# Performance work log

Hardware: AMD Instinct MI355X
Metric: run time of the kernel (lower is better)

The kernel has to match this reference:

```python
import jax, jax.numpy as jnp
import numpy as np

BATCH = 2
SEQ = 2048
DIM = 2048
HEADS = 16
DIM_HEAD = 64
DIM_INNER = HEADS * DIM_HEAD  # 1024
SOFTCAP = 50.0
EPS = 1e-12


def setup_inputs() -> dict:
    key = jax.random.key(0)
    k1, k2, k3, k4 = jax.random.split(key, 4)
    x = jax.random.normal(k1, (BATCH, SEQ, DIM), dtype=jnp.float32)
    # RMSNorm gamma param (initialized near zero in the torch module)
    gamma = jax.random.normal(k2, (DIM,), dtype=jnp.float32) * 0.02
    # Linear weights stored already-transposed: x @ W
    w_qkv = jax.random.normal(k3, (DIM, 3 * DIM_INNER), dtype=jnp.float32) * (DIM ** -0.5)
    w_out = jax.random.normal(k4, (DIM_INNER, DIM), dtype=jnp.float32) * (DIM_INNER ** -0.5)
    # (type, offset, length) triples per batch; bidirectional attention inside each span
    modalities = jnp.array(
        [[[0, 256, 256], [0, 1024, 512]],
         [[0, 128, 256], [0, 1536, 384]]], dtype=jnp.int32)
    return dict(x=x, gamma=gamma, w_qkv=w_qkv, w_out=w_out, modalities=modalities)


def _transfusion_attn_mask(seq_len, modalities):
    # causal | (q in span AND kv in span)  -> Bool[b, i, j]
    seq = jnp.arange(seq_len)
    causal = seq[:, None] >= seq[None, :]                      # [i, j]
    offsets = modalities[..., 1]                                # [b, m]
    ends = offsets + modalities[..., 2]                         # [b, m]
    q_in = seq[None, None, :] >= offsets[..., None]             # [b, m, i]
    kv_in = seq[None, None, :] < ends[..., None]                # [b, m, j]
    is_modality = jnp.any(q_in[..., :, None] & kv_in[..., None, :], axis=1)  # [b, i, j]
    return causal[None] | is_modality


def _rmsnorm(x, gamma):
    n = jnp.sqrt(jnp.sum(x * x, axis=-1, keepdims=True))
    x = x / jnp.maximum(n, EPS)
    return x * (DIM ** 0.5) * (gamma + 1.0)


def reference(x, gamma, w_qkv, w_out, modalities):
    xn = _rmsnorm(x, gamma)
    qkv = xn @ w_qkv                                            # [b, n, 3*h*d]
    qkv = qkv.reshape(BATCH, SEQ, 3, HEADS, DIM_HEAD)
    qkv = jnp.transpose(qkv, (2, 0, 3, 1, 4))                   # [3, b, h, n, d]
    q, k, v = qkv[0], qkv[1], qkv[2]
    q = q * (DIM_HEAD ** -0.5)
    sim = jnp.einsum('bhid,bhjd->bhij', q, k)
    sim = jnp.tanh(sim / SOFTCAP) * SOFTCAP                     # softclamp
    mask = _transfusion_attn_mask(SEQ, modalities)              # [b, i, j]
    neg = -jnp.finfo(sim.dtype).max
    sim = jnp.where(mask[:, None, :, :], sim, neg)
    attn = jax.nn.softmax(sim, axis=-1)
    out = jnp.einsum('bhij,bhjd->bhid', attn, v)
    out = jnp.transpose(out, (0, 2, 1, 3)).reshape(BATCH, SEQ, DIM_INNER)
    return out @ w_out
```

## Files before the change

### kernel.cpp

```cpp
#include <hip/hip_runtime.h>
#include <hip/hip_bf16.h>

typedef unsigned short u16;
typedef unsigned int u32;
typedef __attribute__((ext_vector_type(8))) short short8;
typedef __attribute__((ext_vector_type(4))) float f32x4;
typedef __attribute__((ext_vector_type(4))) u16 u16x4;

#define DEV __device__ __forceinline__

DEV u16 f2bf(float f) {
    union { float f; u32 u; } v; v.f = f;
    u32 r = v.u;
    u32 lsb = (r >> 16) & 1u;
    r += 0x7fffu + lsb;
    return (u16)(r >> 16);
}

DEV void gload_lds16(const u16* g, u16* l) {
    __builtin_amdgcn_global_load_lds(
        (const __attribute__((address_space(1))) u32*)(const void*)g,
        (__attribute__((address_space(3))) u32*)(void*)l,
        16, 0, 0);
}

__global__ void prep(const float* __restrict__ x, const float* __restrict__ gamma,
                     const float* __restrict__ w_qkv, const float* __restrict__ w_out,
                     u16* __restrict__ xn, u16* __restrict__ wqkvT, u16* __restrict__ woutT) {
    __shared__ float tile[32][33];
    __shared__ float red[4];
    int id = blockIdx.x;
    int t = threadIdx.x;
    if (id < 8192) {
        const float* in; u16* out; int R, C, bx, by;
        if (id < 6144) { in = w_qkv; out = wqkvT; R = 2048; C = 3072; bx = id % 96; by = id / 96; }
        else { id -= 6144; in = w_out; out = woutT; R = 1024; C = 2048; bx = id % 64; by = id / 64; }
        int tx = t & 31, ty = t >> 5;
        int c0 = bx * 32, r0 = by * 32;
#pragma unroll
        for (int i = 0; i < 4; i++)
            tile[ty * 4 + i][tx] = in[(size_t)(r0 + ty * 4 + i) * C + c0 + tx];
        __syncthreads();
#pragma unroll
        for (int i = 0; i < 4; i++)
            out[(size_t)(c0 + ty * 4 + i) * R + r0 + tx] = f2bf(tile[tx][ty * 4 + i]);
    } else {
        int row = id - 8192;
        const float4* xr = (const float4*)(x + (size_t)row * 2048);
        float4 a = xr[t];
        float4 b = xr[256 + t];
        float ss = a.x * a.x + a.y * a.y + a.z * a.z + a.w * a.w +
                   b.x * b.x + b.y * b.y + b.z * b.z + b.w * b.w;
#pragma unroll
        for (int off = 32; off; off >>= 1) ss += __shfl_xor(ss, off);
        if ((t & 63) == 0) red[t >> 6] = ss;
        __syncthreads();
        float tot = red[0] + red[1] + red[2] + red[3];
        float n = sqrtf(tot);
        float inv = 45.254833995939045f / fmaxf(n, 1e-12f);
        const float4* gr = (const float4*)gamma;
        float4 g0 = gr[t], g1 = gr[256 + t];
        u16x4 o0 = { f2bf(a.x * inv * (g0.x + 1.f)), f2bf(a.y * inv * (g0.y + 1.f)),
                     f2bf(a.z * inv * (g0.z + 1.f)), f2bf(a.w * inv * (g0.w + 1.f)) };
        u16x4 o1 = { f2bf(b.x * inv * (g1.x + 1.f)), f2bf(b.y * inv * (g1.y + 1.f)),
                     f2bf(b.z * inv * (g1.z + 1.f)), f2bf(b.w * inv * (g1.w + 1.f)) };
        u16x4* xo = (u16x4*)(xn + (size_t)row * 2048);
        xo[t] = o0;
        xo[256 + t] = o1;
    }
}

template <int EPI, int BN>
__global__ __launch_bounds__(512, 4) void gemmw(
    const u16* __restrict__ A, const u16* __restrict__ BT,
    int M, int N, int K,
    float* __restrict__ Cout,
    u16* __restrict__ qb, u16* __restrict__ kb, u16* __restrict__ vT) {
    constexpr int NF = BN / 64;
    constexpr bool BX = (BN * 4) > 512;
    __shared__ __align__(16) u16 As[3][4096];
    __shared__ __align__(16) u16 Bs[3][BN * 32];
    int t = threadIdx.x, lane = t & 63, wid = t >> 6;
    int g = lane >> 4, r = lane & 15;
    int wm = wid >> 2, wn = wid & 3;
    int csw = (r >> 1) & 3;

    int id = blockIdx.x;
    int xcd = id & 7, slot = id >> 3;
    int by = (xcd >> 1) * 8 + (slot >> 3);
    int bx = (xcd & 1) * 8 + (slot & 7);
    int brow = by * 128, bcol = bx * BN;

    int gk = (t & 3) ^ ((t >> 3) & 3);
    const u16* Ag = A + (size_t)(brow + (t >> 2)) * K + gk * 8;
    const u16* Bg = BT + (size_t)(bcol + (t >> 2)) * K + gk * 8;
    const u16* Bg2 = BT + (size_t)(bcol + 128 + (t >> 2)) * K + gk * 8;
    int dst = (t & ~63) * 8;

    f32x4 acc[4][NF] = {};
    short8 areg[4], breg[NF];
    int NT = K >> 5;

#define STG(kt_, b3_) { \
        gload_lds16(Ag + (kt_) * 32, &As[b3_][dst]); \
        gload_lds16(Bg + (kt_) * 32, &Bs[b3_][dst]); \
        if constexpr (BX) { if (t < 256) gload_lds16(Bg2 + (kt_) * 32, &Bs[b3_][4096 + dst]); } }
#define SCHEDB() __builtin_amdgcn_sched_barrier(0)
#define BAR() __builtin_amdgcn_s_barrier()

    STG(0, 0);
    if (NT > 1) STG(1, 1);
    asm volatile("s_waitcnt vmcnt(0)" ::: "memory");
    SCHEDB();
    BAR();

    int c0 = 0;
    for (int kt = 0; kt < NT; ++kt) {
        int c2 = c0 + 2; if (c2 >= 3) c2 -= 3;
        bool s1 = kt + 1 < NT, s2 = kt + 2 < NT;
        if (s2) STG(kt + 2, c2);
        const u16* Ac = As[c0];
        const u16* Bc = Bs[c0];
#pragma unroll
        for (int mf = 0; mf < 4; mf++)
            areg[mf] = *(const short8*)&Ac[(wm * 64 + mf * 16 + r) * 32 + (g ^ csw) * 8];
#pragma unroll
        for (int nf = 0; nf < NF; nf++)
            breg[nf] = *(const short8*)&Bc[(wn * (BN / 4) + nf * 16 + r) * 32 + (g ^ csw) * 8];
        asm volatile("s_waitcnt lgkmcnt(0)" ::: "memory");
        SCHEDB();
        __builtin_amdgcn_s_setprio(1);
#pragma unroll
        for (int mf = 0; mf < 4; mf++)
#pragma unroll
            for (int nf = 0; nf < NF; nf++)
                acc[mf][nf] = __builtin_amdgcn_mfma_f32_16x16x32_bf16(areg[mf], breg[nf], acc[mf][nf], 0, 0, 0);
        __builtin_amdgcn_s_setprio(0);
        if (s2) {
            if (BX && wid < 4) { asm volatile("s_waitcnt vmcnt(3)" ::: "memory"); }
            else               { asm volatile("s_waitcnt vmcnt(2)" ::: "memory"); }
        } else if (s1) {
            asm volatile("s_waitcnt vmcnt(0)" ::: "memory");
        }
        SCHEDB();
        BAR();
        c0 = (c0 + 1 == 3) ? 0 : c0 + 1;
    }
#undef STG
#undef SCHEDB
#undef BAR

    if (EPI == 0) {
#pragma unroll
        for (int mf = 0; mf < 4; mf++)
#pragma unroll
            for (int nf = 0; nf < NF; nf++) {
                int cb = bcol + wn * (BN / 4) + nf * 16 + r;
                int which = cb >> 10;
                int hd = cb & 1023;
                int hh = hd >> 6, d = hd & 63;
#pragma unroll
                for (int j = 0; j < 4; j++) {
                    int rr = brow + wm * 64 + mf * 16 + 4 * g + j;
                    int b = rr >> 11, nn = rr & 2047;
                    float v = acc[mf][nf][j];
                    size_t bh = (size_t)(b * 16 + hh);
                    if (which == 0)      qb[(bh * 2048 + nn) * 64 + d] = f2bf(v * 0.125f);
                    else if (which == 1) kb[(bh * 2048 + nn) * 64 + d] = f2bf(v);
                    else                 vT[(bh * 64 + d) * 2048 + nn] = f2bf(v);
                }
            }
    } else {
#pragma unroll
        for (int mf = 0; mf < 4; mf++)
#pragma unroll
            for (int nf = 0; nf < NF; nf++) {
                int cb = bcol + wn * (BN / 4) + nf * 16 + r;
#pragma unroll
                for (int j = 0; j < 4; j++) {
                    int rr = brow + wm * 64 + mf * 16 + 4 * g + j;
                    Cout[(size_t)rr * N + cb] = acc[mf][nf][j];
                }
            }
    }
}

template <int EPI, int BN, int CCOL>
__global__ __launch_bounds__(512, 1) void gemmcf(
    const u16* __restrict__ A, const u16* __restrict__ BT,
    int M, int N, int K,
    float* __restrict__ Cout,
    u16* __restrict__ qb, u16* __restrict__ kb, u16* __restrict__ vT) {
    constexpr int HN = BN / 2;
    constexpr int NF2 = BN / 64;
    constexpr int NG0 = (NF2 + 1) / 2;
    constexpr bool B2 = (HN * 8) > 512;
    __shared__ __align__(16) u16 As[2][2][8192];
    __shared__ __align__(16) u16 Bs[2][2][HN * 64];
    int t = threadIdx.x, lane = t & 63, wid = t >> 6;
    int g = lane >> 4, r = lane & 15;
    int wm = wid >> 2, wn = wid & 3;
    int bhalf = wn >> 1;
    int cb0w = (wn & 1) * (BN / 4);
    int rsw = r & 7;

    int id = blockIdx.x;
    int xcd = id & 7, slot = id >> 3;
    int by = (xcd >> 1) * 4 + slot / CCOL;
    int bx = (xcd & 1) * CCOL + slot % CCOL;
    int brow = by * 256, bcol = bx * BN;

    int gsl = (t & 7) ^ ((t >> 3) & 7);
    const u16* Ag = A + (size_t)(brow + (t >> 3)) * K + gsl * 8;
    const u16* Bg = BT + (size_t)(bcol + (t >> 3)) * K + gsl * 8;
    int dstc = t * 8;

    f32x4 acc[2][4][NF2] = {};
    short8 areg[4][2], breg[NF2][2];
    int NT = K >> 6;

#define STG_A(bf_, kt_, h_) { \
        gload_lds16(Ag + (size_t)((h_) * 128) * K + (kt_) * 64, &As[bf_][h_][dstc]); \
        gload_lds16(Ag + (size_t)((h_) * 128 + 64) * K + (kt_) * 64, &As[bf_][h_][4096 + dstc]); }
#define STG_B(bf_, kt_, h_) { \
        gload_lds16(Bg + (size_t)((h_) * HN) * K + (kt_) * 64, &Bs[bf_][h_][dstc]); \
        if constexpr (B2) { if (t < 256) \
            gload_lds16(Bg + (size_t)((h_) * HN + 64) * K + (kt_) * 64, &Bs[bf_][h_][4096 + dstc]); } }
#define RD_A(qm_) { \
    _Pragma("unroll") for (int mf = 0; mf < 4; mf++) \
    _Pragma("unroll") for (int ks = 0; ks < 2; ks++) \
        areg[mf][ks] = *(const short8*)&As[buf][qm_][(wm * 64 + mf * 16 + r) * 64 + (((ks << 2) + g) ^ rsw) * 8]; }
#define RD_B() { \
    _Pragma("unroll") for (int nf = 0; nf < NF2; nf++) \
    _Pragma("unroll") for (int ks = 0; ks < 2; ks++) \
        breg[nf][ks] = *(const short8*)&Bs[buf][bhalf][(cb0w + nf * 16 + r) * 64 + (((ks << 2) + g) ^ rsw) * 8]; }
#define MFMA_G(qm_, nf0_, nf1_) { \
    __builtin_amdgcn_s_setprio(1); \
    _Pragma("unroll") for (int ks = 0; ks < 2; ks++) \
    _Pragma("unroll") for (int mf = 0; mf < 4; mf++) \
    _Pragma("unroll") for (int nf = nf0_; nf < nf1_; nf++) \
        acc[qm_][mf][nf] = __builtin_amdgcn_mfma_f32_16x16x32_bf16( \
            areg[mf][ks], breg[nf][ks], acc[qm_][mf][nf], 0, 0, 0); \
    __builtin_amdgcn_s_setprio(0); }
#define SCHEDB() __builtin_amdgcn_sched_barrier(0)
#define BAR() __builtin_amdgcn_s_barrier()

    STG_A(0, 0, 0); STG_A(0, 0, 1); STG_B(0, 0, 0); STG_B(0, 0, 1);
    if (NT > 1) { STG_A(1, 1, 0); STG_A(1, 1, 1); }
    if (NT > 1) { asm volatile("s_waitcnt vmcnt(4)" ::: "memory"); }
    else        { asm volatile("s_waitcnt vmcnt(0)" ::: "memory"); }
    SCHEDB();
    BAR();

    for (int kt = 0; kt < NT; ++kt) {
        int buf = kt & 1, ob = buf ^ 1;
        bool s1 = kt + 1 < NT, s2 = kt + 2 < NT;

        RD_B(); RD_A(0);
        if (s1) STG_B(ob, kt + 1, 1);
        asm volatile("s_waitcnt lgkmcnt(0)" ::: "memory");
        SCHEDB();
        MFMA_G(0, 0, NG0);
        BAR();

        if (s1) STG_B(ob, kt + 1, 0);
        if (s2) STG_A(buf, kt + 2, 0);
        MFMA_G(0, NG0, NF2);
        BAR();

        RD_A(1);
        asm volatile("s_waitcnt lgkmcnt(0)" ::: "memory");
        SCHEDB();
        MFMA_G(1, 0, NG0);
        BAR();

        if (s2) STG_A(buf, kt + 2, 1);
        MFMA_G(1, NG0, NF2);
        if (s2)      { asm volatile("s_waitcnt vmcnt(4)" ::: "memory"); }
        else if (s1) { asm volatile("s_waitcnt vmcnt(0)" ::: "memory"); }
        SCHEDB();
        BAR();
    }
#undef STG_A
#undef STG_B
#undef RD_A
#undef RD_B
#undef MFMA_G
#undef SCHEDB
#undef BAR

    if (EPI == 0) {
#pragma unroll
        for (int qm = 0; qm < 2; qm++)
#pragma unroll
            for (int mf = 0; mf < 4; mf++)
#pragma unroll
                for (int nf = 0; nf < NF2; nf++) {
                    int cb = bcol + bhalf * HN + cb0w + nf * 16 + r;
                    int which = cb >> 10;
                    int hd = cb & 1023;
                    int hh = hd >> 6, d = hd & 63;
#pragma unroll
                    for (int j = 0; j < 4; j++) {
                        int rr = brow + qm * 128 + wm * 64 + mf * 16 + 4 * g + j;
                        int b = rr >> 11, nn = rr & 2047;
                        float v = acc[qm][mf][nf][j];
                        size_t bh = (size_t)(b * 16 + hh);
                        if (which == 0)      qb[(bh * 2048 + nn) * 64 + d] = f2bf(v * 0.125f);
                        else if (which == 1) kb[(bh * 2048 + nn) * 64 + d] = f2bf(v);
                        else                 vT[(bh * 64 + d) * 2048 + nn] = f2bf(v);
                    }
                }
    } else {
#pragma unroll
        for (int qm = 0; qm < 2; qm++)
#pragma unroll
            for (int mf = 0; mf < 4; mf++)
#pragma unroll
                for (int nf = 0; nf < NF2; nf++) {
                    int cb = bcol + bhalf * HN + cb0w + nf * 16 + r;
#pragma unroll
                    for (int j = 0; j < 4; j++) {
                        int rr = brow + qm * 128 + wm * 64 + mf * 16 + 4 * g + j;
                        Cout[(size_t)rr * N + cb] = acc[qm][mf][nf][j];
                    }
                }
    }
}

__global__ __launch_bounds__(256, 3) void flash_attn(
    const u16* __restrict__ q, const u16* __restrict__ kk, const u16* __restrict__ vT,
    const int* __restrict__ mods, u16* __restrict__ attn_out) {
    __shared__ __align__(16) u16 Ks[2][4096];
    __shared__ __align__(16) u16 Vs[2][4096];
    __shared__ __align__(16) u16 Plds[4][16][72];
    int t = threadIdx.x, lane = t & 63, wave = t >> 6;
    int g = lane >> 4, r = lane & 15;
    int h = blockIdx.x, b = blockIdx.y;
    int qs = (31 - blockIdx.z) * 64;
    int bh = b * 16 + h;
    int qbase = qs + wave * 16;

    int off0 = mods[b * 6 + 1], end0 = off0 + mods[b * 6 + 2];
    int off1 = mods[b * 6 + 4], end1 = off1 + mods[b * 6 + 5];

    const u16* Qp = q + ((size_t)bh * 2048 + qbase) * 64;
    short8 qf0 = *(const short8*)(Qp + (size_t)r * 64 + 8 * g);
    short8 qf1 = *(const short8*)(Qp + (size_t)r * 64 + 32 + 8 * g);

    int iq = qbase + r;
    int lim0 = (iq >= off0) ? end0 : 0;
    int lim1 = (iq >= off1) ? end1 : 0;
    int rowlim = max(iq + 1, max(lim0, lim1));

    int jlb = qs + 64;
    if (qs + 63 >= off0) jlb = max(jlb, end0);
    if (qs + 63 >= off1) jlb = max(jlb, end1);

    const u16* Kp = kk + (size_t)bh * 2048 * 64;
    const u16* Vp = vT + (size_t)bh * 64 * 2048;
    u16* Pw = &Plds[wave][0][0];

    f32x4 ot[4] = {};
    float psA = 0.f, psB = 0.f;
    int sw = r & 7;

    auto stage64 = [&](const u16* gbase, int gstride, u16* lds) {
#pragma unroll
        for (int i = 0; i < 2; i++) {
            int c = i * 256 + t;
            int row = c >> 3;
            int gsl = (c & 7) ^ (row & 7);
            gload_lds16(gbase + (size_t)row * gstride + 8 * gsl,
                        lds + (size_t)(c & ~63) * 8);
        }
    };

    stage64(Kp, 64, Ks[0]);
    stage64(Vp, 2048, Vs[0]);
    int buf = 0;

    for (int jb = 0; jb < jlb; jb += 64) {
        if (jb + 64 < jlb) {
            stage64(Kp + (size_t)(jb + 64) * 64, 64, Ks[buf ^ 1]);
            stage64(Vp + (jb + 64), 2048, Vs[buf ^ 1]);
            asm volatile("s_waitcnt vmcnt(4)" ::: "memory");
        } else {
            asm volatile("s_waitcnt vmcnt(0)" ::: "memory");
        }
        __builtin_amdgcn_s_barrier();
        const u16* Kt = Ks[buf];
        const u16* Vt = Vs[buf];

        f32x4 st[4];
#pragma unroll
        for (int tt = 0; tt < 4; tt++) {
            int row = 16 * tt + r;
            short8 kf0 = *(const short8*)&Kt[(size_t)(row * 8 + (g ^ sw)) * 8];
            short8 kf1 = *(const short8*)&Kt[(size_t)(row * 8 + ((4 + g) ^ sw)) * 8];
            f32x4 z = {};
            z = __builtin_amdgcn_mfma_f32_16x16x32_bf16(kf0, qf0, z, 0, 0, 0);
            z = __builtin_amdgcn_mfma_f32_16x16x32_bf16(kf1, qf1, z, 0, 0, 0);
            st[tt] = z;
        }
#pragma unroll
        for (int tt = 0; tt < 4; tt++) {
            int kvb = jb + 16 * tt + 4 * g;
            float p0, p1, p2, p3;
#pragma unroll
            for (int j = 0; j < 4; j++) {
                float x = st[tt][j];
                float x2 = x * x;
                float inner = __builtin_fmaf(x2, 2.1333333e-8f, -1.3333333e-4f);
                float poly = __builtin_fmaf(x2, inner, 1.0f);
                float pv = __expf(x * poly);
                pv = (kvb + j < rowlim) ? pv : 0.f;
                if (j == 0) p0 = pv; else if (j == 1) p1 = pv;
                else if (j == 2) p2 = pv; else p3 = pv;
            }
            psA += p0 + p1;
            psB += p2 + p3;
            u32 pk0, pk1;
            asm("v_cvt_pk_bf16_f32 %0, %1, %2" : "=v"(pk0) : "v"(p0), "v"(p1));
            asm("v_cvt_pk_bf16_f32 %0, %1, %2" : "=v"(pk1) : "v"(p2), "v"(p3));
            *(u32*)&Pw[r * 72 + 16 * tt + 4 * g] = pk0;
            *(u32*)&Pw[r * 72 + 16 * tt + 4 * g + 2] = pk1;
        }
        short8 pf0 = *(const short8*)&Pw[r * 72 + 8 * g];
        short8 pf1 = *(const short8*)&Pw[r * 72 + 32 + 8 * g];
#pragma unroll
        for (int dt = 0; dt < 4; dt++) {
            int row = 16 * dt + r;
            short8 vf0 = *(const short8*)&Vt[(size_t)(row * 8 + (g ^ sw)) * 8];
            short8 vf1 = *(const short8*)&Vt[(size_t)(row * 8 + ((4 + g) ^ sw)) * 8];
            ot[dt] = __builtin_amdgcn_mfma_f32_16x16x32_bf16(vf0, pf0, ot[dt], 0, 0, 0);
            ot[dt] = __builtin_amdgcn_mfma_f32_16x16x32_bf16(vf1, pf1, ot[dt], 0, 0, 0);
        }
        asm volatile("s_waitcnt lgkmcnt(0)" ::: "memory");
        __builtin_amdgcn_s_barrier();
        buf ^= 1;
    }

    float lrow = psA + psB;
    lrow += __shfl_xor(lrow, 16);
    lrow += __shfl_xor(lrow, 32);
    float inv = 1.f / lrow;
    u16* Op = attn_out + ((size_t)(b * 2048 + qbase + r)) * 1024 + h * 64;
#pragma unroll
    for (int dt = 0; dt < 4; dt++) {
        u16x4 o = { f2bf(ot[dt][0] * inv), f2bf(ot[dt][1] * inv),
                    f2bf(ot[dt][2] * inv), f2bf(ot[dt][3] * inv) };
        *(u16x4*)(Op + dt * 16 + 4 * g) = o;
    }
}

extern "C" void kernel_launch(void* const* d_in, const int* in_sizes, int n_in,
                              void* d_out, int out_size, void* d_ws, size_t ws_size,
                              hipStream_t stream) {
    const float* x = (const float*)d_in[0];
    const float* gamma = (const float*)d_in[1];
    const float* w_qkv = (const float*)d_in[2];
    const float* w_out = (const float*)d_in[3];
    const int* mods = (const int*)d_in[4];
    float* out = (float*)d_out;

    u16* ws = (u16*)d_ws;
    u16* xn    = ws;
    u16* wqkvT = ws + 8388608;
    u16* woutT = ws + 14680064;
    u16* qb    = ws + 16777216;
    u16* kb    = ws + 20971520;
    u16* vT    = ws + 25165824;
    u16* ao    = ws + 29360128;

    prep<<<dim3(12288), dim3(256), 0, stream>>>(x, gamma, w_qkv, w_out, xn, wqkvT, woutT);
    gemmw<0, 192><<<dim3(512), dim3(512), 0, stream>>>(xn, wqkvT, 4096, 3072, 2048,
                                                       nullptr, qb, kb, vT);
    flash_attn<<<dim3(16, 2, 32), dim3(256), 0, stream>>>(qb, kb, vT, mods, ao);
    gemmcf<1, 128, 8><<<dim3(256), dim3(512), 0, stream>>>(ao, woutT, 4096, 2048, 1024,
                                                           out, nullptr, nullptr, nullptr);
}
```

Before: 166.2 us.

## Process two 16-row query subtiles per wave to reuse K/V fragments in attention

Each wave now handles 32 query rows instead of 16, so a block covers 128 query rows and the grid halves along the query axis. Every K and V fragment read from LDS is used for two MFMA subtiles, which halves the K/V LDS traffic and the global staging per query row. The cost is more registers per thread (two sets of accumulators and Q fragments), which may lower occupancy, and fewer blocks (512), which reduces parallelism and coarsens the causal tail so some masked KV work is wasted.

```diff
diff --git a/kernel.cpp b/kernel.cpp
--- a/kernel.cpp
+++ b/kernel.cpp
@@ -333,36 +333,43 @@
     const int* __restrict__ mods, u16* __restrict__ attn_out) {
     __shared__ __align__(16) u16 Ks[2][4096];
     __shared__ __align__(16) u16 Vs[2][4096];
-    __shared__ __align__(16) u16 Plds[4][16][72];
+    __shared__ __align__(16) u16 Plds[4][2][16][72];
     int t = threadIdx.x, lane = t & 63, wave = t >> 6;
     int g = lane >> 4, r = lane & 15;
     int h = blockIdx.x, b = blockIdx.y;
-    int qs = (31 - blockIdx.z) * 64;
+    int qs = (15 - blockIdx.z) * 128;
     int bh = b * 16 + h;
-    int qbase = qs + wave * 16;
+    int qbase = qs + wave * 32;
 
     int off0 = mods[b * 6 + 1], end0 = off0 + mods[b * 6 + 2];
     int off1 = mods[b * 6 + 4], end1 = off1 + mods[b * 6 + 5];
 
     const u16* Qp = q + ((size_t)bh * 2048 + qbase) * 64;
-    short8 qf0 = *(const short8*)(Qp + (size_t)r * 64 + 8 * g);
-    short8 qf1 = *(const short8*)(Qp + (size_t)r * 64 + 32 + 8 * g);
-
-    int iq = qbase + r;
-    int lim0 = (iq >= off0) ? end0 : 0;
-    int lim1 = (iq >= off1) ? end1 : 0;
-    int rowlim = max(iq + 1, max(lim0, lim1));
-
-    int jlb = qs + 64;
-    if (qs + 63 >= off0) jlb = max(jlb, end0);
-    if (qs + 63 >= off1) jlb = max(jlb, end1);
+    short8 qf0[2], qf1[2];
+#pragma unroll
+    for (int s = 0; s < 2; s++) {
+        qf0[s] = *(const short8*)(Qp + (size_t)(s * 16 + r) * 64 + 8 * g);
+        qf1[s] = *(const short8*)(Qp + (size_t)(s * 16 + r) * 64 + 32 + 8 * g);
+    }
+
+    int rowlim[2];
+#pragma unroll
+    for (int s = 0; s < 2; s++) {
+        int iq = qbase + s * 16 + r;
+        int lim0 = (iq >= off0) ? end0 : 0;
+        int lim1 = (iq >= off1) ? end1 : 0;
+        rowlim[s] = max(iq + 1, max(lim0, lim1));
+    }
+
+    int jlb = qs + 128;
+    if (qs + 127 >= off0) jlb = max(jlb, end0);
+    if (qs + 127 >= off1) jlb = max(jlb, end1);
 
     const u16* Kp = kk + (size_t)bh * 2048 * 64;
     const u16* Vp = vT + (size_t)bh * 64 * 2048;
-    u16* Pw = &Plds[wave][0][0];
-
-    f32x4 ot[4] = {};
-    float psA = 0.f, psB = 0.f;
+
+    f32x4 ot[2][4] = {};
+    float psA[2] = {}, psB[2] = {};
     int sw = r & 7;
 
     auto stage64 = [&](const u16* gbase, int gstride, u16* lds) {
@@ -392,65 +399,82 @@
         const u16* Kt = Ks[buf];
         const u16* Vt = Vs[buf];
 
-        f32x4 st[4];
+        f32x4 st[2][4];
 #pragma unroll
         for (int tt = 0; tt < 4; tt++) {
             int row = 16 * tt + r;
             short8 kf0 = *(const short8*)&Kt[(size_t)(row * 8 + (g ^ sw)) * 8];
             short8 kf1 = *(const short8*)&Kt[(size_t)(row * 8 + ((4 + g) ^ sw)) * 8];
-            f32x4 z = {};
-            z = __builtin_amdgcn_mfma_f32_16x16x32_bf16(kf0, qf0, z, 0, 0, 0);
-            z = __builtin_amdgcn_mfma_f32_16x16x32_bf16(kf1, qf1, z, 0, 0, 0);
-            st[tt] = z;
-        }
-#pragma unroll
-        for (int tt = 0; tt < 4; tt++) {
-            int kvb = jb + 16 * tt + 4 * g;
-            float p0, p1, p2, p3;
-#pragma unroll
-            for (int j = 0; j < 4; j++) {
-                float x = st[tt][j];
-                float x2 = x * x;
-                float inner = __builtin_fmaf(x2, 2.1333333e-8f, -1.3333333e-4f);
-                float poly = __builtin_fmaf(x2, inner, 1.0f);
-                float pv = __expf(x * poly);
-                pv = (kvb + j < rowlim) ? pv : 0.f;
-                if (j == 0) p0 = pv; else if (j == 1) p1 = pv;
-                else if (j == 2) p2 = pv; else p3 = pv;
+#pragma unroll
+            for (int s = 0; s < 2; s++) {
+                f32x4 z = {};
+                z = __builtin_amdgcn_mfma_f32_16x16x32_bf16(kf0, qf0[s], z, 0, 0, 0);
+                z = __builtin_amdgcn_mfma_f32_16x16x32_bf16(kf1, qf1[s], z, 0, 0, 0);
+                st[s][tt] = z;
             }
-            psA += p0 + p1;
-            psB += p2 + p3;
-            u32 pk0, pk1;
-            asm("v_cvt_pk_bf16_f32 %0, %1, %2" : "=v"(pk0) : "v"(p0), "v"(p1));
-            asm("v_cvt_pk_bf16_f32 %0, %1, %2" : "=v"(pk1) : "v"(p2), "v"(p3));
-            *(u32*)&Pw[r * 72 + 16 * tt + 4 * g] = pk0;
-            *(u32*)&Pw[r * 72 + 16 * tt + 4 * g + 2] = pk1;
-        }
-        short8 pf0 = *(const short8*)&Pw[r * 72 + 8 * g];
-        short8 pf1 = *(const short8*)&Pw[r * 72 + 32 + 8 * g];
+        }
+#pragma unroll
+        for (int s = 0; s < 2; s++) {
+            u16* Pws = &Plds[wave][s][0][0];
+#pragma unroll
+            for (int tt = 0; tt < 4; tt++) {
+                int kvb = jb + 16 * tt + 4 * g;
+                float p0, p1, p2, p3;
+#pragma unroll
+                for (int j = 0; j < 4; j++) {
+                    float x = st[s][tt][j];
+                    float x2 = x * x;
+                    float inner = __builtin_fmaf(x2, 2.1333333e-8f, -1.3333333e-4f);
+                    float poly = __builtin_fmaf(x2, inner, 1.0f);
+                    float pv = __expf(x * poly);
+                    pv = (kvb + j < rowlim[s]) ? pv : 0.f;
+                    if (j == 0) p0 = pv; else if (j == 1) p1 = pv;
+                    else if (j == 2) p2 = pv; else p3 = pv;
+                }
+                psA[s] += p0 + p1;
+                psB[s] += p2 + p3;
+                u32 pk0, pk1;
+                asm("v_cvt_pk_bf16_f32 %0, %1, %2" : "=v"(pk0) : "v"(p0), "v"(p1));
+                asm("v_cvt_pk_bf16_f32 %0, %1, %2" : "=v"(pk1) : "v"(p2), "v"(p3));
+                *(u32*)&Pws[r * 72 + 16 * tt + 4 * g] = pk0;
+                *(u32*)&Pws[r * 72 + 16 * tt + 4 * g + 2] = pk1;
+            }
+        }
+        short8 pf0[2], pf1[2];
+#pragma unroll
+        for (int s = 0; s < 2; s++) {
+            pf0[s] = *(const short8*)&Plds[wave][s][r][8 * g];
+            pf1[s] = *(const short8*)&Plds[wave][s][r][32 + 8 * g];
+        }
 #pragma unroll
         for (int dt = 0; dt < 4; dt++) {
             int row = 16 * dt + r;
             short8 vf0 = *(const short8*)&Vt[(size_t)(row * 8 + (g ^ sw)) * 8];
             short8 vf1 = *(const short8*)&Vt[(size_t)(row * 8 + ((4 + g) ^ sw)) * 8];
-            ot[dt] = __builtin_amdgcn_mfma_f32_16x16x32_bf16(vf0, pf0, ot[dt], 0, 0, 0);
-            ot[dt] = __builtin_amdgcn_mfma_f32_16x16x32_bf16(vf1, pf1, ot[dt], 0, 0, 0);
+#pragma unroll
+            for (int s = 0; s < 2; s++) {
+                ot[s][dt] = __builtin_amdgcn_mfma_f32_16x16x32_bf16(vf0, pf0[s], ot[s][dt], 0, 0, 0);
+                ot[s][dt] = __builtin_amdgcn_mfma_f32_16x16x32_bf16(vf1, pf1[s], ot[s][dt], 0, 0, 0);
+            }
         }
         asm volatile("s_waitcnt lgkmcnt(0)" ::: "memory");
         __builtin_amdgcn_s_barrier();
         buf ^= 1;
     }
 
-    float lrow = psA + psB;
-    lrow += __shfl_xor(lrow, 16);
-    lrow += __shfl_xor(lrow, 32);
-    float inv = 1.f / lrow;
-    u16* Op = attn_out + ((size_t)(b * 2048 + qbase + r)) * 1024 + h * 64;
-#pragma unroll
-    for (int dt = 0; dt < 4; dt++) {
-        u16x4 o = { f2bf(ot[dt][0] * inv), f2bf(ot[dt][1] * inv),
-                    f2bf(ot[dt][2] * inv), f2bf(ot[dt][3] * inv) };
-        *(u16x4*)(Op + dt * 16 + 4 * g) = o;
+#pragma unroll
+    for (int s = 0; s < 2; s++) {
+        float lrow = psA[s] + psB[s];
+        lrow += __shfl_xor(lrow, 16);
+        lrow += __shfl_xor(lrow, 32);
+        float inv = 1.f / lrow;
+        u16* Op = attn_out + ((size_t)(b * 2048 + qbase + s * 16 + r)) * 1024 + h * 64;
+#pragma unroll
+        for (int dt = 0; dt < 4; dt++) {
+            u16x4 o = { f2bf(ot[s][dt][0] * inv), f2bf(ot[s][dt][1] * inv),
+                        f2bf(ot[s][dt][2] * inv), f2bf(ot[s][dt][3] * inv) };
+            *(u16x4*)(Op + dt * 16 + 4 * g) = o;
+        }
     }
 }
 
@@ -476,7 +500,7 @@
     prep<<<dim3(12288), dim3(256), 0, stream>>>(x, gamma, w_qkv, w_out, xn, wqkvT, woutT);
     gemmw<0, 192><<<dim3(512), dim3(512), 0, stream>>>(xn, wqkvT, 4096, 3072, 2048,
                                                        nullptr, qb, kb, vT);
-    flash_attn<<<dim3(16, 2, 32), dim3(256), 0, stream>>>(qb, kb, vT, mods, ao);
+    flash_attn<<<dim3(16, 2, 16), dim3(256), 0, stream>>>(qb, kb, vT, mods, ao);
     gemmcf<1, 128, 8><<<dim3(256), dim3(512), 0, stream>>>(ao, woutT, 4096, 2048, 1024,
                                                            out, nullptr, nullptr, nullptr);
 }
```

Measured after the change: 177.0 us. 6.5% more time.
